# Kernel optimization log

Measured on AMD Instinct MI355X. Metric: run time of the kernel, lower is better.

## Reference

```python
import jax, jax.numpy as jnp
import numpy as np

N, T, CIN, H, L, NC = 64, 150, 150, 1024, 3, 60
EPS = 1e-5


def setup_inputs() -> dict:
    key = jax.random.key(0)
    ks = jax.random.split(key, 12)
    s = 0.05
    return {
        "x": jax.random.normal(ks[0], (N, T, CIN), jnp.float32),
        "bn_gamma": jnp.ones((CIN,), jnp.float32),
        "bn_beta": jnp.zeros((CIN,), jnp.float32),
        "w_ih0": jax.random.normal(ks[1], (2, 3 * H, CIN), jnp.float32) * s,
        "w_hh0": jax.random.normal(ks[2], (2, 3 * H, H), jnp.float32) * s,
        "b_ih0": jax.random.normal(ks[3], (2, 3 * H), jnp.float32) * s,
        "b_hh0": jax.random.normal(ks[4], (2, 3 * H), jnp.float32) * s,
        "w_ih": jax.random.normal(ks[5], (L - 1, 2, 3 * H, 2 * H), jnp.float32) * s,
        "w_hh": jax.random.normal(ks[6], (L - 1, 2, 3 * H, H), jnp.float32) * s,
        "b_ih": jax.random.normal(ks[7], (L - 1, 2, 3 * H), jnp.float32) * s,
        "b_hh": jax.random.normal(ks[8], (L - 1, 2, 3 * H), jnp.float32) * s,
        "fc_w": jax.random.normal(ks[9], (NC, 2 * H), jnp.float32) * s,
        "fc_b": jax.random.normal(ks[10], (NC,), jnp.float32) * s,
    }


def _bigru_layer(x, w_ih, w_hh, b_ih, b_hh):
    # x: [T, N, I]. Faithful to the source's per-timestep loop: BOTH directions
    # scan forward in time (the 'reverse' direction never sees a reversed seq,
    # since the original feeds length-1 slices while carrying hidden state).
    # Precompute input projections for the whole sequence: [T, 2, N, 3H]
    gi = jnp.einsum('tni,dgi->tdng', x, w_ih) + b_ih[None, :, None, :]

    def step(h, gi_t):
        # h: [2, N, H], gi_t: [2, N, 3H]
        gh = jnp.einsum('dnh,dgh->dng', h, w_hh) + b_hh[:, None, :]
        r = jax.nn.sigmoid(gi_t[..., :H] + gh[..., :H])
        z = jax.nn.sigmoid(gi_t[..., H:2 * H] + gh[..., H:2 * H])
        n = jnp.tanh(gi_t[..., 2 * H:] + r * gh[..., 2 * H:])
        h_new = (1.0 - z) * n + z * h
        out = jnp.concatenate([h_new[0], h_new[1]], axis=-1)  # [N, 2H]
        return h_new, out

    h0 = jnp.zeros((2, x.shape[1], H), x.dtype)
    _, outs = jax.lax.scan(step, h0, gi)
    return outs  # [T, N, 2H]


def reference(x, bn_gamma, bn_beta, w_ih0, w_hh0, b_ih0, b_hh0,
              w_ih, w_hh, b_ih, b_hh, fc_w, fc_b):
    # BatchNorm1d over channels, train mode: batch stats over (N, T), biased var.
    mean = x.mean(axis=(0, 1))
    var = x.var(axis=(0, 1))
    xn = (x - mean) * jax.lax.rsqrt(var + EPS) * bn_gamma + bn_beta

    h = jnp.transpose(xn, (1, 0, 2))  # [T, N, CIN]
    h = _bigru_layer(h, w_ih0, w_hh0, b_ih0, b_hh0)
    for l in range(L - 1):  # small fixed layer loop
        h = _bigru_layer(h, w_ih[l], w_hh[l], b_ih[l], b_hh[l])

    # seq_len == T for every sample, so the gathered hidden is the last step.
    last = h[-1]  # [N, 2H]
    return last @ fc_w.T + fc_b  # [N, num_class]
```

## Files before the change

### kernel.cpp

```cpp
#include <hip/hip_runtime.h>
#include <math.h>

#define NB   64
#define TT   150
#define CIN  150
#define HH   1024
#define G3   3072
#define NCOL 6144
#define KP0  160
#define RT   9600
#define NC   60
#define NSLOT 151
#define SLOT_STRIDE 66560

using bf16x8 = __attribute__((ext_vector_type(8))) __bf16;
using f32x4  = __attribute__((ext_vector_type(4))) float;

static __device__ __forceinline__ unsigned short f2bf(float f){
  unsigned int x = __builtin_bit_cast(unsigned int, f);
  x += 0x7fffu + ((x >> 16) & 1u);
  return (unsigned short)(x >> 16);
}
static __device__ __forceinline__ float bf2f(unsigned short u){
  unsigned int x = ((unsigned int)u) << 16;
  return __builtin_bit_cast(float, x);
}
static __device__ __forceinline__ float sigmoidf(float x){
  return 1.0f / (1.0f + expf(-x));
}

static __device__ __forceinline__ void gload16(const void* g, void* l){
  __builtin_amdgcn_global_load_lds(
      (const __attribute__((address_space(1))) void*)g,
      (__attribute__((address_space(3))) void*)l, 16, 0, 0);
}

__global__ void bn_stats(const float* __restrict__ x, const float* __restrict__ gamma,
                         const float* __restrict__ beta, float* __restrict__ ss){
  const int c = blockIdx.x;
  float s = 0.f, s2 = 0.f;
  for (int i = threadIdx.x; i < RT; i += 256){
    float v = x[(size_t)i * CIN + c];
    s += v; s2 += v * v;
  }
  __shared__ float sh1[256], sh2[256];
  sh1[threadIdx.x] = s; sh2[threadIdx.x] = s2;
  __syncthreads();
  for (int st = 128; st > 0; st >>= 1){
    if ((int)threadIdx.x < st){
      sh1[threadIdx.x] += sh1[threadIdx.x + st];
      sh2[threadIdx.x] += sh2[threadIdx.x + st];
    }
    __syncthreads();
  }
  if (threadIdx.x == 0){
    float mean = sh1[0] * (1.f / RT);
    float var  = sh2[0] * (1.f / RT) - mean * mean;
    float sc   = rsqrtf(var + 1e-5f) * gamma[c];
    ss[c]       = sc;
    ss[CIN + c] = beta[c] - mean * sc;
  }
}

__global__ void bn_apply(const float* __restrict__ x, const float* __restrict__ ss,
                         unsigned short* __restrict__ xn){
  int idx = blockIdx.x * 256 + threadIdx.x;
  if (idx >= RT * KP0) return;
  int r = idx / KP0, c = idx - r * KP0;
  int t = r >> 6, n = r & 63;
  float v = 0.f;
  if (c < CIN) v = x[((size_t)n * TT + t) * CIN + c] * ss[c] + ss[CIN + c];
  xn[idx] = f2bf(v);
}

__global__ void cast_bf(const float* __restrict__ s, unsigned short* __restrict__ d, int n){
  for (int i = blockIdx.x * 256 + threadIdx.x; i < n; i += gridDim.x * 256)
    d[i] = f2bf(s[i]);
}

__global__ void cast_pad_w0(const float* __restrict__ w, unsigned short* __restrict__ d){
  int idx = blockIdx.x * 256 + threadIdx.x;
  if (idx >= NCOL * KP0) return;
  int row = idx / KP0, c = idx - row * KP0;
  d[idx] = (c < CIN) ? f2bf(w[(size_t)row * CIN + c]) : (unsigned short)0;
}

__global__ void zero16(uint4* p, int n){
  int i = blockIdx.x * 256 + threadIdx.x;
  if (i < n) p[i] = make_uint4(0u, 0u, 0u, 0u);
}

__global__ void guard_k(float* out){ out[0] = -12345.0f; }

__global__ __launch_bounds__(256) void gemm_tile(
    const unsigned short* __restrict__ A, const unsigned short* __restrict__ B,
    const float* __restrict__ bias, unsigned short* __restrict__ C, int K)
{
  const int r0 = blockIdx.x * 128;
  const int c0 = blockIdx.y * 128;
  const int tid = threadIdx.x;
  const int wid = tid >> 6;
  const int l   = tid & 63;
  const int lr  = l & 15;
  const int lk  = (l >> 4) * 8;
  const int wm  = wid >> 1;
  const int wn  = wid & 1;

  __shared__ unsigned short As[128 * 32];
  __shared__ unsigned short Bs[128 * 32];

  const int c1   = wid * 64 + l;
  const int rowS = c1 >> 2;
  const int ccS  = c1 & 3;

  f32x4 acc[4][4];
#pragma unroll
  for (int i = 0; i < 4; ++i)
#pragma unroll
    for (int j = 0; j < 4; ++j) acc[i][j] = f32x4{0,0,0,0};

  const unsigned short* Ag0 = A + (size_t)(r0 + rowS) * K + ccS * 8;
  const unsigned short* Ag1 = A + (size_t)(r0 + 64 + rowS) * K + ccS * 8;
  const unsigned short* Bg0 = B + (size_t)(c0 + rowS) * K + ccS * 8;
  const unsigned short* Bg1 = B + (size_t)(c0 + 64 + rowS) * K + ccS * 8;
  unsigned short* As0 = As + wid * 512;
  unsigned short* As1 = As + 2048 + wid * 512;
  unsigned short* Bs0 = Bs + wid * 512;
  unsigned short* Bs1 = Bs + 2048 + wid * 512;

  for (int k0 = 0; k0 < K; k0 += 32){
    gload16(Ag0 + k0, As0);
    gload16(Ag1 + k0, As1);
    gload16(Bg0 + k0, Bs0);
    gload16(Bg1 + k0, Bs1);
    __syncthreads();

    bf16x8 af[4], bfr[4];
#pragma unroll
    for (int mt = 0; mt < 4; ++mt)
      af[mt] = *(const bf16x8*)(As + (wm * 64 + mt * 16 + lr) * 32 + lk);
#pragma unroll
    for (int nt = 0; nt < 4; ++nt)
      bfr[nt] = *(const bf16x8*)(Bs + (wn * 64 + nt * 16 + lr) * 32 + lk);
#pragma unroll
    for (int mt = 0; mt < 4; ++mt)
#pragma unroll
      for (int nt = 0; nt < 4; ++nt)
        acc[mt][nt] = __builtin_amdgcn_mfma_f32_16x16x32_bf16(af[mt], bfr[nt], acc[mt][nt], 0, 0, 0);
    __syncthreads();
  }

  const int rb = (l >> 4) * 4;
#pragma unroll
  for (int mt = 0; mt < 4; ++mt){
#pragma unroll
    for (int nt = 0; nt < 4; ++nt){
      const int col = c0 + wn * 64 + nt * 16 + lr;
      const float bv = bias[col];
#pragma unroll
      for (int reg = 0; reg < 4; ++reg){
        const int row = r0 + wm * 64 + mt * 16 + rb + reg;
        C[(size_t)row * NCOL + col] = f2bf(acc[mt][nt][reg] + bv);
      }
    }
  }
}

__global__ __launch_bounds__(1024, 1) void gru_layer(
    const unsigned short* __restrict__ whh,
    const float* __restrict__ bhh,
    const unsigned short* __restrict__ gi,
    unsigned short* __restrict__ outb,
    float* __restrict__ hfinal,
    unsigned short* __restrict__ hbig,
    int* __restrict__ flags, int wout)
{
  const int d  = blockIdx.x >> 6;
  const int jt = blockIdx.x & 63;
  const int j0 = jt * 16;
  const int tid = threadIdx.x;
  const int w  = tid >> 6;
  const int wq = w & 3;
  const int kq = w >> 2;
  const int l  = tid & 63;
  const int lr = l & 15;
  const int hi = l >> 4;

  __shared__ unsigned char wlds[98304];
  __shared__ f32x4 red4[2304];

  {
    const unsigned short* wsrc = whh + (size_t)d * (G3 * HH);
    for (int c = tid; c < 6144; c += 1024){
      int g   = c >> 11;
      int rem = c & 2047;
      int r   = rem >> 7;
      int kc  = rem & 127;
      uint4 v = *(const uint4*)(wsrc + (size_t)(g * HH + j0 + r) * HH + kc * 8);
      int kcs = (kc & ~7) | ((kc + r) & 7);
      *(uint4*)(wlds + g * 32768 + r * 2048 + kcs * 16) = v;
    }
  }
  __syncthreads();

  float4 br4 = make_float4(0, 0, 0, 0), bz4 = br4, bn4 = br4;
  if (kq == 0){
    br4 = *(const float4*)(bhh + d * G3 +          j0 + hi * 4);
    bz4 = *(const float4*)(bhh + d * G3 + HH +     j0 + hi * 4);
    bn4 = *(const float4*)(bhh + d * G3 + 2 * HH + j0 + hi * 4);
  }

  const int n    = wq * 16 + lr;
  const int jcol = j0 + hi * 4;

  unsigned short* dirbase = hbig + (size_t)d * NSLOT * SLOT_STRIDE;
  int* ctr = &flags[d * 64];

  float hold[4] = {0.f, 0.f, 0.f, 0.f};

  for (int t = 0; t < TT; ++t){
    const unsigned short* hprev = dirbase + (size_t)t * SLOT_STRIDE;
    unsigned short*       hnext = dirbase + (size_t)(t + 1) * SLOT_STRIDE;

    ushort4 gr4, gz4, gn4;
    if (kq == 0){
      size_t gbase = (size_t)(t * NB + n) * NCOL + (size_t)d * G3 + jcol;
      gr4 = *(const ushort4*)(gi + gbase);
      gz4 = *(const ushort4*)(gi + gbase + HH);
      gn4 = *(const ushort4*)(gi + gbase + 2 * HH);
    }

    if (t){
      if (tid == 0){
        const int tgt = 64 * t;
        int cap = 0;
        while (__hip_atomic_load(ctr, __ATOMIC_RELAXED, __HIP_MEMORY_SCOPE_AGENT) < tgt){
          if (++cap > 20000000) break;
          __builtin_amdgcn_s_sleep(1);
        }
      }
      __syncthreads();
    }

    f32x4 ar = {0,0,0,0}, az = {0,0,0,0}, an = {0,0,0,0};
    const unsigned short* hrow = hprev + (size_t)n * HH + kq * 256 + hi * 8;

    bf16x8 ha[8];
#pragma unroll
    for (int i = 0; i < 8; ++i) ha[i] = *(const bf16x8*)(hrow + i * 32);

#pragma unroll
    for (int i = 0; i < 8; ++i){
      const int kc  = kq * 32 + i * 4 + hi;
      const int kcs = (kc & ~7) | ((kc + lr) & 7);
      const int off = lr * 2048 + kcs * 16;
      bf16x8 a_r = *(const bf16x8*)(wlds +          off);
      bf16x8 a_z = *(const bf16x8*)(wlds + 32768 +  off);
      bf16x8 a_n = *(const bf16x8*)(wlds + 65536 +  off);
      ar = __builtin_amdgcn_mfma_f32_16x16x32_bf16(a_r, ha[i], ar, 0, 0, 0);
      az = __builtin_amdgcn_mfma_f32_16x16x32_bf16(a_z, ha[i], az, 0, 0, 0);
      an = __builtin_amdgcn_mfma_f32_16x16x32_bf16(a_n, ha[i], an, 0, 0, 0);
    }

    __syncthreads();
    if (kq > 0){
      const int src = (kq - 1) * 4 + wq;
      red4[(src * 3 + 0) * 64 + l] = ar;
      red4[(src * 3 + 1) * 64 + l] = az;
      red4[(src * 3 + 2) * 64 + l] = an;
    }
    __syncthreads();

    if (kq == 0){
#pragma unroll
      for (int kqp = 1; kqp < 4; ++kqp){
        const int src = (kqp - 1) * 4 + wq;
        ar += red4[(src * 3 + 0) * 64 + l];
        az += red4[(src * 3 + 1) * 64 + l];
        an += red4[(src * 3 + 2) * 64 + l];
      }

      ushort4 hb_;
      const float* br = (const float*)&br4;
      const float* bz = (const float*)&bz4;
      const float* bn_ = (const float*)&bn4;
      const unsigned short* g_r = (const unsigned short*)&gr4;
      const unsigned short* g_z = (const unsigned short*)&gz4;
      const unsigned short* g_n = (const unsigned short*)&gn4;
#pragma unroll
      for (int reg = 0; reg < 4; ++reg){
        float r  = sigmoidf(bf2f(g_r[reg]) + ar[reg] + br[reg]);
        float z  = sigmoidf(bf2f(g_z[reg]) + az[reg] + bz[reg]);
        float nn = tanhf(bf2f(g_n[reg]) + r * (an[reg] + bn_[reg]));
        hold[reg] = (1.f - z) * nn + z * hold[reg];
      }
      hb_.x = f2bf(hold[0]); hb_.y = f2bf(hold[1]);
      hb_.z = f2bf(hold[2]); hb_.w = f2bf(hold[3]);
      __hip_atomic_store((unsigned long long*)(hnext + (size_t)n * HH + jcol),
                         __builtin_bit_cast(unsigned long long, hb_),
                         __ATOMIC_RELAXED, __HIP_MEMORY_SCOPE_AGENT);
      if (wout)
        *(ushort4*)(outb + (size_t)(t * NB + n) * (2 * HH) + (size_t)d * HH + jcol) = hb_;
      if (t == TT - 1)
        *(float4*)(hfinal + (size_t)(d * NB + n) * HH + jcol) =
            make_float4(hold[0], hold[1], hold[2], hold[3]);
    }

    __syncthreads();
    if (tid == 0)
      __hip_atomic_fetch_add(ctr, 1, __ATOMIC_RELEASE, __HIP_MEMORY_SCOPE_AGENT);
  }
}

__global__ void fc_kernel(const float* __restrict__ hf, const float* __restrict__ fw,
                          const float* __restrict__ fb, float* __restrict__ out){
  int b = blockIdx.x;
  int n = b / NC, c = b - n * NC;
  int l = threadIdx.x;
  float s = 0.f;
  for (int k = l; k < 2 * HH; k += 64){
    float hv = (k < HH) ? hf[(size_t)n * HH + k]
                        : hf[(size_t)(NB + n) * HH + (k - HH)];
    s += hv * fw[(size_t)c * (2 * HH) + k];
  }
#pragma unroll
  for (int off = 32; off > 0; off >>= 1) s += __shfl_down(s, off);
  if (l == 0) out[n * NC + c] = s + fb[c];
}

extern "C" void kernel_launch(void* const* d_in, const int* in_sizes, int n_in,
                              void* d_out, int out_size, void* d_ws, size_t ws_size,
                              hipStream_t stream)
{
  const float* x      = (const float*)d_in[0];
  const float* gamma  = (const float*)d_in[1];
  const float* beta   = (const float*)d_in[2];
  const float* w_ih0  = (const float*)d_in[3];
  const float* w_hh0  = (const float*)d_in[4];
  const float* b_ih0  = (const float*)d_in[5];
  const float* b_hh0  = (const float*)d_in[6];
  const float* w_ih   = (const float*)d_in[7];
  const float* w_hh   = (const float*)d_in[8];
  const float* b_ih   = (const float*)d_in[9];
  const float* b_hh   = (const float*)d_in[10];
  const float* fc_w   = (const float*)d_in[11];
  const float* fc_b   = (const float*)d_in[12];
  float* out = (float*)d_out;

  char* ws = (char*)d_ws;
  size_t off = 0;
  auto alloc = [&](size_t bytes)->void*{
    void* p = ws + off; off += (bytes + 255) & ~(size_t)255; return p;
  };
  unsigned short* whh_bf = (unsigned short*)alloc((size_t)3 * 2 * G3 * HH * 2);
  unsigned short* w0_bf  = (unsigned short*)alloc((size_t)NCOL * KP0 * 2);
  unsigned short* wih_bf = (unsigned short*)alloc((size_t)2 * NCOL * 2 * HH * 2);
  unsigned short* xn_bf  = (unsigned short*)alloc((size_t)RT * KP0 * 2);
  unsigned short* gi_bf  = (unsigned short*)alloc((size_t)RT * NCOL * 2);
  unsigned short* out0   = (unsigned short*)alloc((size_t)RT * 2 * HH * 2);
  unsigned short* out1   = (unsigned short*)alloc((size_t)RT * 2 * HH * 2);
  float* hfinal = (float*)alloc((size_t)2 * NB * HH * 4);
  unsigned short* hbig = (unsigned short*)alloc((size_t)2 * NSLOT * SLOT_STRIDE * 2);
  float* ss = (float*)alloc(2048);
  int* flags = (int*)alloc(1024);

  if (off > ws_size){ guard_k<<<1, 1, 0, stream>>>(out); return; }

  bn_stats<<<CIN, 256, 0, stream>>>(x, gamma, beta, ss);
  bn_apply<<<(RT * KP0 + 255) / 256, 256, 0, stream>>>(x, ss, xn_bf);
  cast_pad_w0<<<(NCOL * KP0 + 255) / 256, 256, 0, stream>>>(w_ih0, w0_bf);
  cast_bf<<<4096, 256, 0, stream>>>(w_hh0, whh_bf, 2 * G3 * HH);
  cast_bf<<<4096, 256, 0, stream>>>(w_hh,  whh_bf + (size_t)2 * G3 * HH, 2 * 2 * G3 * HH);
  cast_bf<<<4096, 256, 0, stream>>>(w_ih,  wih_bf, 2 * NCOL * 2 * HH);

  zero16<<<32, 256, 0, stream>>>((uint4*)hbig, NB * HH * 2 / 16);
  zero16<<<32, 256, 0, stream>>>((uint4*)(hbig + (size_t)NSLOT * SLOT_STRIDE),
                                 NB * HH * 2 / 16);

  for (int lyr = 0; lyr < 3; ++lyr){
    if (lyr == 0){
      gemm_tile<<<dim3(RT / 128, NCOL / 128), 256, 0, stream>>>(xn_bf, w0_bf, b_ih0, gi_bf, KP0);
    } else {
      const unsigned short* Ain = (lyr == 1) ? out0 : out1;
      gemm_tile<<<dim3(RT / 128, NCOL / 128), 256, 0, stream>>>(
          Ain, wih_bf + (size_t)(lyr - 1) * NCOL * 2 * HH,
          b_ih + (size_t)(lyr - 1) * NCOL, gi_bf, 2 * HH);
    }
    zero16<<<1, 32, 0, stream>>>((uint4*)flags, 512 / 16);

    const unsigned short* whh_l = whh_bf + (size_t)lyr * 2 * G3 * HH;
    const float* bhh_l = (lyr == 0) ? b_hh0 : (b_hh + (size_t)(lyr - 1) * NCOL);
    unsigned short* outb = (lyr == 0) ? out0 : out1;
    int wout = (lyr < 2) ? 1 : 0;
    gru_layer<<<128, 1024, 0, stream>>>(whh_l, bhh_l, gi_bf, outb,
                                        hfinal, hbig, flags, wout);
  }
  fc_kernel<<<NB * NC, 64, 0, stream>>>(hfinal, fc_w, fc_b, out);
}
```

Baseline: 5.490 ms.

## Overlap next layer's input projection with GRU recurrence via extra producer blocks

Result: slower. 15.67 ms (+185.5%).

```diff
diff --git a/kernel.cpp b/kernel.cpp
--- a/kernel.cpp
+++ b/kernel.cpp
@@ -166,28 +166,72 @@
   }
 }
 
-__global__ __launch_bounds__(1024, 1) void gru_layer(
+__global__ __launch_bounds__(1024, 1) void fused_layer(
     const unsigned short* __restrict__ whh,
     const float* __restrict__ bhh,
-    const unsigned short* __restrict__ gi,
+    unsigned short* __restrict__ gi,
     unsigned short* __restrict__ outb,
     float* __restrict__ hfinal,
     unsigned short* __restrict__ hbig,
-    int* __restrict__ flags, int wout)
+    int* __restrict__ flags, int wout,
+    const unsigned short* __restrict__ wih_next,
+    const float* __restrict__ bih_next,
+    int do_next)
 {
+  __shared__ unsigned char wlds[98304];
+  __shared__ f32x4 red4[2304];
+
+  const int tid = threadIdx.x;
+  const int w  = tid >> 6;
+  const int l  = tid & 63;
+  const int lr = l & 15;
+  const int hi = l >> 4;
+
+  if (blockIdx.x >= 128){
+    if (!do_next) return;
+    if (w >= 12) return;
+    const int wk = blockIdx.x - 128;
+    const int rt = w >> 2;
+    const int rtile = w / 3;
+    const int ctile = w - rtile * 3;
+    const int c0 = wk * 48 + ctile * 16;
+    const int lk = hi * 8;
+    (void)rt;
+    const float bv = bih_next[c0 + lr];
+    int* ctr0 = &flags[0];
+    int* ctr1 = &flags[64];
+    const int rb = hi * 4;
+
+    for (int t = 0; t < TT; ++t){
+      const int tgt = 64 * (t + 1);
+      int cap = 0;
+      while (__hip_atomic_load(ctr0, __ATOMIC_RELAXED, __HIP_MEMORY_SCOPE_AGENT) < tgt ||
+             __hip_atomic_load(ctr1, __ATOMIC_RELAXED, __HIP_MEMORY_SCOPE_AGENT) < tgt){
+        if (++cap > 50000000) break;
+        __builtin_amdgcn_s_sleep(2);
+      }
+      const unsigned short* Arow = outb + (size_t)(t * 64 + rtile * 16 + lr) * (2 * HH) + lk;
+      const unsigned short* Brow = wih_next + (size_t)(c0 + lr) * (2 * HH) + lk;
+      f32x4 acc = {0, 0, 0, 0};
+      for (int k0 = 0; k0 < 2 * HH; k0 += 32){
+        bf16x8 a = *(const bf16x8*)(Arow + k0);
+        bf16x8 b = *(const bf16x8*)(Brow + k0);
+        acc = __builtin_amdgcn_mfma_f32_16x16x32_bf16(a, b, acc, 0, 0, 0);
+      }
+#pragma unroll
+      for (int reg = 0; reg < 4; ++reg){
+        const int row = t * 64 + rtile * 16 + rb + reg;
+        gi[(size_t)row * NCOL + c0 + lr] = f2bf(acc[reg] + bv);
+      }
+    }
+    return;
+  }
+
   const int d  = blockIdx.x >> 6;
   const int jt = blockIdx.x & 63;
   const int j0 = jt * 16;
-  const int tid = threadIdx.x;
-  const int w  = tid >> 6;
   const int wq = w & 3;
   const int kq = w >> 2;
-  const int l  = tid & 63;
-  const int lr = l & 15;
-  const int hi = l >> 4;
-
-  __shared__ unsigned char wlds[98304];
-  __shared__ f32x4 red4[2304];
 
   {
     const unsigned short* wsrc = whh + (size_t)d * (G3 * HH);
@@ -300,7 +344,10 @@
                          __builtin_bit_cast(unsigned long long, hb_),
                          __ATOMIC_RELAXED, __HIP_MEMORY_SCOPE_AGENT);
       if (wout)
-        *(ushort4*)(outb + (size_t)(t * NB + n) * (2 * HH) + (size_t)d * HH + jcol) = hb_;
+        __hip_atomic_store((unsigned long long*)(outb + (size_t)(t * NB + n) * (2 * HH)
+                                                 + (size_t)d * HH + jcol),
+                           __builtin_bit_cast(unsigned long long, hb_),
+                           __ATOMIC_RELAXED, __HIP_MEMORY_SCOPE_AGENT);
       if (t == TT - 1)
         *(float4*)(hfinal + (size_t)(d * NB + n) * HH + jcol) =
             make_float4(hold[0], hold[1], hold[2], hold[3]);
@@ -377,23 +424,23 @@
   zero16<<<32, 256, 0, stream>>>((uint4*)(hbig + (size_t)NSLOT * SLOT_STRIDE),
                                  NB * HH * 2 / 16);
 
+  gemm_tile<<<dim3(RT / 128, NCOL / 128), 256, 0, stream>>>(xn_bf, w0_bf, b_ih0, gi_bf, KP0);
+
   for (int lyr = 0; lyr < 3; ++lyr){
-    if (lyr == 0){
-      gemm_tile<<<dim3(RT / 128, NCOL / 128), 256, 0, stream>>>(xn_bf, w0_bf, b_ih0, gi_bf, KP0);
-    } else {
-      const unsigned short* Ain = (lyr == 1) ? out0 : out1;
-      gemm_tile<<<dim3(RT / 128, NCOL / 128), 256, 0, stream>>>(
-          Ain, wih_bf + (size_t)(lyr - 1) * NCOL * 2 * HH,
-          b_ih + (size_t)(lyr - 1) * NCOL, gi_bf, 2 * HH);
-    }
     zero16<<<1, 32, 0, stream>>>((uint4*)flags, 512 / 16);
 
     const unsigned short* whh_l = whh_bf + (size_t)lyr * 2 * G3 * HH;
     const float* bhh_l = (lyr == 0) ? b_hh0 : (b_hh + (size_t)(lyr - 1) * NCOL);
-    unsigned short* outb = (lyr == 0) ? out0 : out1;
+    unsigned short* outb = (lyr == 1) ? out1 : out0;
     int wout = (lyr < 2) ? 1 : 0;
-    gru_layer<<<128, 1024, 0, stream>>>(whh_l, bhh_l, gi_bf, outb,
-                                        hfinal, hbig, flags, wout);
+    int do_next = (lyr < 2) ? 1 : 0;
+    const unsigned short* wih_next = wih_bf + (size_t)lyr * NCOL * (2 * HH);
+    const float* bih_next = b_ih + (size_t)lyr * NCOL;
+    fused_layer<<<256, 1024, 0, stream>>>(whh_l, bhh_l, gi_bf, outb,
+                                          hfinal, hbig, flags, wout,
+                                          (lyr < 2) ? wih_next : wih_bf,
+                                          (lyr < 2) ? bih_next : fc_b,
+                                          do_next);
   }
   fc_kernel<<<NB * NC, 64, 0, stream>>>(hfinal, fc_w, fc_b, out);
 }
```
